# Kernel optimization log

Measured on AMD Instinct MI355X. Metric: run time of the kernel, lower is better.

Reference implementation:

```python
import jax, jax.numpy as jnp
import numpy as np

K = 3          # hypergraph neighbors (hardcoded self.kn = 3)
H = 3          # attention heads (hardcoded num_heads=3)
QKD = 32       # qkv_dim
BN_EPS = 1e-5


def _pe(channels, num_frames):
    # Ter_Embed: sinusoidal over frame index, constant across joints -> (1,C,T,1)
    pos = jnp.arange(num_frames, dtype=jnp.float32)
    div = jnp.exp(jnp.arange(0, channels, 2, dtype=jnp.float32) * (-np.log(10000.0) / channels))
    ang = pos[:, None] * div[None, :]                      # (T, C/2)
    pe = jnp.zeros((num_frames, channels), jnp.float32)
    pe = pe.at[:, 0::2].set(jnp.sin(ang)).at[:, 1::2].set(jnp.cos(ang))
    return pe.T[None, :, :, None]                          # (1,C,T,1)


def _bn(x, g, b):
    # training-mode BatchNorm2d over (N,T,V) per channel
    mu = x.mean(axis=(0, 2, 3), keepdims=True)
    var = x.var(axis=(0, 2, 3), keepdims=True)
    return (x - mu) * jax.lax.rsqrt(var + BN_EPS) * g[None, :, None, None] + b[None, :, None, None]


def setup_inputs() -> dict:
    key = jax.random.key(0)
    ks = jax.random.split(key, 16)
    N, C, T, V = 8, 128, 64, 204
    s = 0.05
    inp = {
        'x': jax.random.normal(ks[0], (N, C, T, V), jnp.float32),
        # Transform.conv1: Conv1d(k, k*k, C, groups=k) -> weight (k*k, 1, C)
        'trans_w': jax.random.normal(ks[1], (K * K, C), jnp.float32) * s,
        'trans_b': jax.random.normal(ks[2], (K * K,), jnp.float32) * s,
        # VertexConv.convK1: Conv1d(k, 1, 1)
        'convk_w': jax.random.normal(ks[3], (K,), jnp.float32) * s,
        'convk_b': jax.random.normal(ks[4], (1,), jnp.float32) * s,
        # to_qkvs: Conv2d(C, 2*H*QKD, 1)
        'qkv_w': jax.random.normal(ks[5], (2 * H * QKD, C), jnp.float32) * s,
        'qkv_b': jax.random.normal(ks[6], (2 * H * QKD,), jnp.float32) * s,
        'alphas': jnp.ones((1, H, 1, 1), jnp.float32),
        'att1s': jnp.broadcast_to(jnp.eye(T, dtype=jnp.float32), (1, H, T, T)) + 0.0,
        # out_nets: Conv2d(H*C, C, (1,1)) + BN
        'out_w': jax.random.normal(ks[7], (C, H * C), jnp.float32) * s,
        'out_b': jax.random.normal(ks[8], (C,), jnp.float32) * s,
        'out_g': jnp.ones((C,), jnp.float32) + jax.random.normal(ks[9], (C,), jnp.float32) * 0.01,
        'out_beta': jax.random.normal(ks[10], (C,), jnp.float32) * 0.01,
        # ff_net: Conv2d(C, C, 1) + BN
        'ff_w': jax.random.normal(ks[11], (C, C), jnp.float32) * s,
        'ff_b': jax.random.normal(ks[12], (C,), jnp.float32) * s,
        'ff_g': jnp.ones((C,), jnp.float32) + jax.random.normal(ks[13], (C,), jnp.float32) * 0.01,
        'ff_beta': jax.random.normal(ks[14], (C,), jnp.float32) * 0.01,
    }
    return inp


def reference(x, trans_w, trans_b, convk_w, convk_b, qkv_w, qkv_b, alphas, att1s,
              out_w, out_b, out_g, out_beta, ff_w, ff_b, ff_g, ff_beta):
    N, C, T, V = x.shape
    orign = x
    # ---------- hypergraph_knn (ssa) ----------
    # cos_dis: F.normalize over last dim (V) then contract c,t -> (N,V,V)
    nrm = jnp.linalg.norm(x, axis=-1, keepdims=True)
    xn = x / jnp.maximum(nrm, 1e-12)
    dis = jnp.einsum('nctu,nctv->nuv', xn, xn)
    _, idx = jax.lax.top_k(dis, K)                                   # (N,V,K)
    # gather neighbor feats: feats[n,c,t,v,k] = x[n,c,t,idx[n,v,k]]
    feats = jnp.take_along_axis(x[:, :, :, None, :], idx[:, None, None, :, :], axis=4)  # (N,C,T,V,K)
    # Transform: grouped Conv1d over C, group g -> K outputs
    m = feats.mean(axis=2).transpose(0, 2, 3, 1)                     # (N,V,K,C)
    mult = jnp.einsum('nvgc,gpc->nvgp', m, trans_w.reshape(K, K, C)) + trans_b.reshape(K, K)
    mult = jax.nn.softmax(mult, axis=-1)                             # (N,V,K,K)
    transformed = jnp.einsum('nctvk,nvkp->nctvp', feats, mult)
    # convK1 pools K -> 1
    pooled = jnp.einsum('nctvk,k->nctv', transformed, convk_w) + convk_b[0]
    x = jax.nn.relu(pooled + orign)
    # ---------- TTA_Block_att ----------
    xs = x + _pe(C, T)
    qkv = jnp.einsum('oc,nctv->notv', qkv_w, xs) + qkv_b[None, :, None, None]
    qkv = qkv.reshape(N, 2 * H, QKD, T, V)
    q, k = qkv[:, :H], qkv[:, H:]
    att = jnp.tanh(jnp.einsum('nhctv,nhcqv->nhtq', q, k) / (QKD * V)) * alphas + att1s  # (N,H,T,T)
    xs2 = jnp.einsum('nctv,nstq->nscqv', x, att).reshape(N, H * C, T, V)
    out = jnp.einsum('os,nstv->notv', out_w, xs2) + out_b[None, :, None, None]
    out = _bn(out, out_g, out_beta)
    xs3 = jax.nn.leaky_relu(out + x, 0.1)                            # ress is identity (in==out)
    ff = jnp.einsum('oc,nctv->notv', ff_w, xs3) + ff_b[None, :, None, None]
    ff = _bn(ff, ff_g, ff_beta)
    return jax.nn.leaky_relu(ff + x, 0.1)
```

## Files before the change

### kernel.cpp

```cpp
#include <hip/hip_runtime.h>
#include <math.h>

#define N_ 8
#define C_ 128
#define T_ 64
#define V_ 204
#define H_ 3
#define QKD_ 32
#define O2_ 192
#define TV_ 13056
#define CT_ 8192
#define TT_ 4096
#define VV_ 41616
#define NCTV_ 13369344ull
#define DSPLIT_ 32
#define ZR_ 208
#define NBLK_ 1632

typedef __attribute__((ext_vector_type(8))) short short8v;
typedef __attribute__((ext_vector_type(4))) float f32x4;

__device__ inline unsigned short bf16rnd(float f) {
  union { float f; unsigned u; } x; x.f = f;
  return (unsigned short)((x.u + 0x7FFFu + ((x.u >> 16) & 1u)) >> 16);
}
__device__ inline float bf2f(unsigned short u) {
  union { unsigned u; float f; } x; x.u = ((unsigned)u) << 16;
  return x.f;
}

__global__ void k_wprep(const float* __restrict__ qw, const float* __restrict__ ow,
                        const float* __restrict__ fw, unsigned short* __restrict__ wb) {
  int g = blockIdx.x * 256 + threadIdx.x;
  if (g >= 704 * 16) return;
  int row = g >> 4, ch = g & 15;
  const float* src;
  if (row < 192) src = qw + row * 128;
  else if (row < 576) { int r = row - 192; src = ow + (r & 127) * 384 + (r >> 7) * 128; }
  else src = fw + (row - 576) * 128;
  f32x4 a = *(const f32x4*)(src + ch * 8);
  f32x4 b = *(const f32x4*)(src + ch * 8 + 4);
  unsigned short buf[8];
  buf[0] = bf16rnd(a.x); buf[1] = bf16rnd(a.y); buf[2] = bf16rnd(a.z); buf[3] = bf16rnd(a.w);
  buf[4] = bf16rnd(b.x); buf[5] = bf16rnd(b.y); buf[6] = bf16rnd(b.z); buf[7] = bf16rnd(b.w);
  *(uint4*)(wb + (size_t)row * 128 + ch * 8) = *(const uint4*)buf;
}

__global__ void k_qkvpe(const float* __restrict__ qw, const float* __restrict__ qb,
                        float* __restrict__ qpe) {
  __shared__ float pes[C_ * T_];
  int tid = threadIdx.x;
  for (int i = tid; i < C_ * T_; i += 256) {
    int t = i & 63, c = i >> 6;
    int j = c >> 1;
    float dv = expf((2.0f * j) * (-logf(10000.0f) / (float)C_));
    float ang = (float)t * dv;
    pes[i] = (c & 1) ? cosf(ang) : sinf(ang);
  }
  __syncthreads();
  int g = blockIdx.x * 256 + tid;
  int t = g & 63, m = g >> 6;
  float a = 0.f;
  for (int c = 0; c < C_; ++c) a += qw[m * C_ + c] * pes[c * T_ + t];
  qpe[g] = a + qb[m];
}

__global__ void k_scale(const float* __restrict__ x, float* __restrict__ s) {
  int gid = blockIdx.x * blockDim.x + threadIdx.x;
  int w = gid >> 6, lane = gid & 63;
  if (w >= N_ * CT_) return;
  const f32x4* row = (const f32x4*)(x + (size_t)w * V_);
  float a = 0.f;
  for (int v4 = lane; v4 < 51; v4 += 64) {
    f32x4 t = row[v4];
    a += t.x * t.x + t.y * t.y + t.z * t.z + t.w * t.w;
  }
#pragma unroll
  for (int off = 32; off >= 1; off >>= 1) a += __shfl_down(a, off, 64);
  if (lane == 0) {
    float d = fmaxf(sqrtf(a), 1e-12f);
    s[w] = 1.0f / (d * d);
  }
}

__global__ __launch_bounds__(256) void k_zprep(const float* __restrict__ x,
                                               const float* __restrict__ s,
                                               unsigned short* __restrict__ zhi,
                                               unsigned short* __restrict__ zlo,
                                               float* __restrict__ cm) {
  int kt = blockIdx.x, ut = blockIdx.y, n = blockIdx.z;
  int k0 = kt * 64, u0 = ut * 64;
  __shared__ float Ts[64][65];
  __shared__ float sq[64];
  int tid = threadIdx.x;
  int uu = tid & 63, kk = tid >> 6;
  int u = u0 + uu;
  bool uok = u < V_;
  const float* xb = x + (size_t)n * CT_ * V_;
#pragma unroll
  for (int it = 0; it < 16; ++it) {
    int kr = kk + it * 4;
    Ts[kr][uu] = uok ? xb[(size_t)(k0 + kr) * V_ + u] : 0.f;
  }
  if (tid < 64) sq[tid] = sqrtf(s[(size_t)n * CT_ + k0 + tid]);
  __syncthreads();
  if (tid < 64 && uok) {
    float a = 0.f;
    for (int t = 0; t < 64; ++t) a += Ts[t][tid];
    cm[((size_t)n * C_ + kt) * V_ + u] = a * (1.0f / 64.0f);
  }
#pragma unroll
  for (int it = 0; it < 4; ++it) {
    int sl = tid + it * 256;
    int u_l = sl & 63, oct = (sl >> 6) & 7, half = sl >> 9;
    int ug = u0 + u_l;
    if (ug >= ZR_) continue;
    unsigned short buf[8];
    if (ug < V_) {
#pragma unroll
      for (int j = 0; j < 8; ++j) {
        float z = Ts[oct * 8 + j][u_l] * sq[oct * 8 + j];
        unsigned short h = bf16rnd(z);
        buf[j] = half ? bf16rnd(z - bf2f(h)) : h;
      }
    } else {
#pragma unroll
      for (int j = 0; j < 8; ++j) buf[j] = 0;
    }
    unsigned short* dst = (half ? zlo : zhi) +
                          (((size_t)n * 1024 + kt * 8 + oct) * ZR_ + ug) * 8;
    *(uint4*)dst = *(const uint4*)buf;
  }
}

__global__ __launch_bounds__(256) void k_dism(const unsigned short* __restrict__ zhi,
                                              const unsigned short* __restrict__ zlo,
                                              float* __restrict__ pdis) {
  int q = blockIdx.x, sp = blockIdx.y, n = blockIdx.z;
  int bu = (q == 2) ? 1 : 0, bv = (q == 0) ? 0 : 1;
  int u0 = bu * 128, v0 = bv * 128;
  bool dg = (bu == bv);
  __shared__ unsigned short As[8 * 128 * 8];
  __shared__ unsigned short Bs[8 * 128 * 8];
  int tid = threadIdx.x, lane = tid & 63, wid = tid >> 6;
  int lr = lane & 15, lg = lane >> 4;
  f32x4 acc[2][8];
#pragma unroll
  for (int mi = 0; mi < 2; ++mi)
#pragma unroll
    for (int li = 0; li < 8; ++li) acc[mi][li] = (f32x4){0.f, 0.f, 0.f, 0.f};
  const int KCH = CT_ / DSPLIT_;
  int kbase = sp * KCH, kend = kbase + KCH;
  for (int kk = kbase; kk < kend; kk += 32) {
    int koct = kk >> 3;
    __syncthreads();
#pragma unroll
    for (int it = 0; it < 4; ++it) {
      int sl = tid + it * 256;
      int row = sl & 127, hs = sl >> 7;
      int slot = hs & 3, half = hs >> 2;
      const unsigned short* src = half ? zlo : zhi;
      size_t ob = ((size_t)n * 1024 + koct + slot) * ZR_;
      int ra = u0 + row; ra = ra > 207 ? 207 : ra;
      *(uint4*)&As[(hs * 128 + row) * 8] = *(const uint4*)(src + (ob + ra) * 8);
      if (!dg) {
        int rb = v0 + row; rb = rb > 207 ? 207 : rb;
        *(uint4*)&Bs[(hs * 128 + row) * 8] = *(const uint4*)(src + (ob + rb) * 8);
      }
    }
    __syncthreads();
    const unsigned short* Bp = dg ? As : Bs;
    short8v ah[2], al[2];
#pragma unroll
    for (int mi = 0; mi < 2; ++mi) {
      int r = wid * 32 + mi * 16 + lr;
      ah[mi] = *(const short8v*)&As[(lg * 128 + r) * 8];
      al[mi] = *(const short8v*)&As[((4 + lg) * 128 + r) * 8];
    }
#pragma unroll
    for (int li = 0; li < 8; ++li) {
      int rv = li * 16 + lr;
      short8v bh = *(const short8v*)&Bp[(lg * 128 + rv) * 8];
      short8v bl = *(const short8v*)&Bp[((4 + lg) * 128 + rv) * 8];
#pragma unroll
      for (int mi = 0; mi < 2; ++mi) {
        acc[mi][li] = __builtin_amdgcn_mfma_f32_16x16x32_bf16(ah[mi], bh, acc[mi][li], 0, 0, 0);
        acc[mi][li] = __builtin_amdgcn_mfma_f32_16x16x32_bf16(ah[mi], bl, acc[mi][li], 0, 0, 0);
        acc[mi][li] = __builtin_amdgcn_mfma_f32_16x16x32_bf16(al[mi], bh, acc[mi][li], 0, 0, 0);
      }
    }
  }
  float* pb = pdis + ((size_t)sp * N_ + n) * VV_;
#pragma unroll
  for (int mi = 0; mi < 2; ++mi) {
#pragma unroll
    for (int li = 0; li < 8; ++li) {
      int v = v0 + li * 16 + lr;
      if (v >= V_) continue;
#pragma unroll
      for (int rr = 0; rr < 4; ++rr) {
        int u = u0 + wid * 32 + mi * 16 + lg * 4 + rr;
        if (u >= V_) continue;
        float val = acc[mi][li][rr];
        pb[(size_t)u * V_ + v] = val;
        if (!dg) pb[(size_t)v * V_ + u] = val;
      }
    }
  }
}

__global__ void k_topk2(const float* __restrict__ pdis, int* __restrict__ idx) {
  int r = blockIdx.x;
  int n = r / V_, u = r - n * V_;
  int lane = threadIdx.x;
  float m0 = -INFINITY, m1 = -INFINITY, m2 = -INFINITY;
  int i0 = 0x7fffffff, i1 = 0x7fffffff, i2 = 0x7fffffff;
#pragma unroll
  for (int g = 0; g < 4; ++g) {
    int v = g * 64 + lane;
    if (v >= V_) break;
    float a = 0.f;
#pragma unroll
    for (int sp = 0; sp < DSPLIT_; ++sp)
      a += pdis[((size_t)sp * N_ + n) * VV_ + (size_t)u * V_ + v];
    if (a > m0 || (a == m0 && v < i0)) {
      m2 = m1; i2 = i1; m1 = m0; i1 = i0; m0 = a; i0 = v;
    } else if (a > m1 || (a == m1 && v < i1)) {
      m2 = m1; i2 = i1; m1 = a; i1 = v;
    } else if (a > m2 || (a == m2 && v < i2)) {
      m2 = a; i2 = v;
    }
  }
#pragma unroll
  for (int msk = 1; msk < 64; msk <<= 1) {
    float o0 = __shfl_xor(m0, msk, 64), o1 = __shfl_xor(m1, msk, 64),
          o2 = __shfl_xor(m2, msk, 64);
    int p0 = __shfl_xor(i0, msk, 64), p1 = __shfl_xor(i1, msk, 64),
        p2 = __shfl_xor(i2, msk, 64);
    float ov[3] = {o0, o1, o2};
    int op[3] = {p0, p1, p2};
#pragma unroll
    for (int e = 0; e < 3; ++e) {
      float a = ov[e]; int v = op[e];
      if (a > m0 || (a == m0 && v < i0)) {
        m2 = m1; i2 = i1; m1 = m0; i1 = i0; m0 = a; i0 = v;
      } else if (a > m1 || (a == m1 && v < i1)) {
        m2 = m1; i2 = i1; m1 = a; i1 = v;
      } else if (a > m2 || (a == m2 && v < i2)) {
        m2 = a; i2 = v;
      }
    }
  }
  if (lane == 0) {
    idx[r * 3 + 0] = i0; idx[r * 3 + 1] = i1; idx[r * 3 + 2] = i2;
  }
}

__global__ void k_w2(const float* __restrict__ cm, const int* __restrict__ idx,
                     const float* __restrict__ tw, const float* __restrict__ tb,
                     const float* __restrict__ ckw, float* __restrict__ w2) {
  int r = blockIdx.x;
  int n = r / V_;
  int lane = threadIdx.x;
  __shared__ float mv[3][C_];
  const int* ib = idx + r * 3;
  int j0 = ib[0], j1 = ib[1], j2 = ib[2];
  const float* cmn = cm + (size_t)n * C_ * V_;
  for (int c = lane; c < C_; c += 64) {
    mv[0][c] = cmn[c * V_ + j0];
    mv[1][c] = cmn[c * V_ + j1];
    mv[2][c] = cmn[c * V_ + j2];
  }
  __syncthreads();
  float p[9];
#pragma unroll
  for (int gp = 0; gp < 9; ++gp) p[gp] = 0.f;
  for (int c = lane; c < C_; c += 64) {
#pragma unroll
    for (int g = 0; g < 3; ++g) {
      float m = mv[g][c];
#pragma unroll
      for (int pp = 0; pp < 3; ++pp) p[g * 3 + pp] += m * tw[(g * 3 + pp) * C_ + c];
    }
  }
#pragma unroll
  for (int off = 32; off >= 1; off >>= 1) {
#pragma unroll
    for (int gp = 0; gp < 9; ++gp) p[gp] += __shfl_down(p[gp], off, 64);
  }
  if (lane == 0) {
    float c0 = ckw[0], c1 = ckw[1], c2 = ckw[2];
#pragma unroll
    for (int g = 0; g < 3; ++g) {
      float m0 = p[g * 3 + 0] + tb[g * 3 + 0];
      float m1 = p[g * 3 + 1] + tb[g * 3 + 1];
      float m2 = p[g * 3 + 2] + tb[g * 3 + 2];
      float mx = fmaxf(m0, fmaxf(m1, m2));
      float e0 = expf(m0 - mx), e1 = expf(m1 - mx), e2 = expf(m2 - mx);
      float inv = 1.0f / (e0 + e1 + e2);
      w2[r * 3 + g] = (e0 * c0 + e1 * c1 + e2 * c2) * inv;
    }
  }
}

__global__ __launch_bounds__(256) void k_x1p(const float* __restrict__ x,
                                             const int* __restrict__ idx,
                                             const float* __restrict__ w2,
                                             const float* __restrict__ ckb,
                                             float* __restrict__ x1p,
                                             unsigned short* __restrict__ x1pb) {
  int t = blockIdx.x, ct = blockIdx.y, n = blockIdx.z;
  int c0 = ct * 32;
  __shared__ float Ts[32][209];
  __shared__ int iw[V_ * 3];
  __shared__ float ww[V_ * 3];
  int tid = threadIdx.x;
  const float* xb = x + ((size_t)n * C_ + c0) * TV_ + t * V_;
  for (int i = tid; i < 32 * V_; i += 256) {
    int c = i / V_, v = i - c * V_;
    Ts[c][v] = xb[(size_t)c * TV_ + v];
  }
  for (int i = tid; i < V_ * 3; i += 256) {
    iw[i] = idx[(size_t)n * V_ * 3 + i];
    ww[i] = w2[(size_t)n * V_ * 3 + i];
  }
  __syncthreads();
  float cb = ckb[0];
  for (int i = tid; i < 32 * V_; i += 256) {
    int v = i >> 5, cl = i & 31;
    int b = v * 3;
    float pooled = Ts[cl][iw[b]] * ww[b] + Ts[cl][iw[b + 1]] * ww[b + 1] +
                   Ts[cl][iw[b + 2]] * ww[b + 2] + cb;
    float val = fmaxf(pooled + Ts[cl][v], 0.f);
    size_t o = ((size_t)(n * V_ + v) * T_ + t) * C_ + c0 + cl;
    x1p[o] = val;
    x1pb[o] = bf16rnd(val);
  }
}

template <int MCH, int OBF, int STATS>
__global__ __launch_bounds__(256) void k_gmm2(const unsigned short* __restrict__ Wb,
                                              const unsigned short* __restrict__ Xp,
                                              const float* __restrict__ addv,
                                              void* __restrict__ Yv,
                                              float* __restrict__ part) {
  int l0 = blockIdx.x * 128, n = blockIdx.z;
  __shared__ unsigned short Xs[128 * 136];
  __shared__ unsigned short Ys[64 * 128];
  int tid = threadIdx.x, lane = tid & 63, wid = tid >> 6;
  int wm = wid >> 1, wl = wid & 1;
  int lr = lane & 15, lg = lane >> 4;
  const unsigned short* xb = Xp + ((size_t)n * TV_ + l0) * 128;
#pragma unroll
  for (int it = 0; it < 8; ++it) {
    int g = tid + it * 256;
    int row = g >> 4, ch = g & 15;
    *(uint4*)&Xs[row * 136 + ch * 8] = *(const uint4*)(xb + (size_t)row * 128 + ch * 8);
  }
  __syncthreads();
  for (int mc = 0; mc < MCH; ++mc) {
    short8v a[2][4];
#pragma unroll
    for (int mi = 0; mi < 2; ++mi) {
      int m = mc * 64 + wm * 32 + mi * 16 + lr;
#pragma unroll
      for (int ks = 0; ks < 4; ++ks)
        a[mi][ks] = *(const short8v*)(Wb + (size_t)m * 128 + ks * 32 + lg * 8);
    }
    f32x4 acc[2][4];
#pragma unroll
    for (int mi = 0; mi < 2; ++mi)
#pragma unroll
      for (int li = 0; li < 4; ++li) acc[mi][li] = (f32x4){0.f, 0.f, 0.f, 0.f};
#pragma unroll
    for (int ks = 0; ks < 4; ++ks) {
#pragma unroll
      for (int li = 0; li < 4; ++li) {
        short8v b = *(const short8v*)&Xs[(wl * 64 + li * 16 + lr) * 136 + ks * 32 + lg * 8];
#pragma unroll
        for (int mi = 0; mi < 2; ++mi)
          acc[mi][li] = __builtin_amdgcn_mfma_f32_16x16x32_bf16(a[mi][ks], b, acc[mi][li], 0, 0, 0);
      }
    }
    if (OBF) {
      __syncthreads();
#pragma unroll
      for (int mi = 0; mi < 2; ++mi)
#pragma unroll
        for (int li = 0; li < 4; ++li) {
          int lloc = wl * 64 + li * 16 + lr;
          int tt = (l0 + lloc) & 63;
#pragma unroll
          for (int r = 0; r < 4; ++r) {
            int mloc = wm * 32 + mi * 16 + lg * 4 + r;
            float val = acc[mi][li][r] + addv[(mc * 64 + mloc) * 64 + tt];
            Ys[mloc * 128 + lloc] = bf16rnd(val);
          }
        }
      __syncthreads();
      unsigned short* Yh = (unsigned short*)Yv;
#pragma unroll
      for (int it = 0; it < 4; ++it) {
        int g = tid + it * 256;
        int row = g >> 4, ch = g & 15;
        *(uint4*)(Yh + ((size_t)n * O2_ + mc * 64 + row) * TV_ + l0 + ch * 8) =
            *(const uint4*)&Ys[row * 128 + ch * 8];
      }
    } else {
      float* Yf = (float*)Yv;
      float st1[2][4] = {}, st2[2][4] = {};
#pragma unroll
      for (int mi = 0; mi < 2; ++mi)
#pragma unroll
        for (int li = 0; li < 4; ++li) {
          int lp = l0 + wl * 64 + li * 16 + lr;
          int m = mc * 64 + wm * 32 + mi * 16 + lg * 4;
          f32x4 o;
#pragma unroll
          for (int r = 0; r < 4; ++r) {
            o[r] = acc[mi][li][r] + addv[m + r];
            if (STATS) { st1[mi][r] += o[r]; st2[mi][r] += o[r] * o[r]; }
          }
          *(f32x4*)(Yf + ((size_t)n * TV_ + lp) * 128 + m) = o;
        }
      if (STATS) {
        int blk2 = ((n * gridDim.x + blockIdx.x) * 2 + wl) * 256;
#pragma unroll
        for (int mi = 0; mi < 2; ++mi)
#pragma unroll
          for (int r = 0; r < 4; ++r) {
            float a1 = st1[mi][r], a2 = st2[mi][r];
            a1 += __shfl_xor(a1, 1, 64); a2 += __shfl_xor(a2, 1, 64);
            a1 += __shfl_xor(a1, 2, 64); a2 += __shfl_xor(a2, 2, 64);
            a1 += __shfl_xor(a1, 4, 64); a2 += __shfl_xor(a2, 4, 64);
            a1 += __shfl_xor(a1, 8, 64); a2 += __shfl_xor(a2, 8, 64);
            if (lr == 0) {
              int m = mc * 64 + wm * 32 + mi * 16 + lg * 4 + r;
              part[blk2 + m] = a1;
              part[blk2 + 128 + m] = a2;
            }
          }
      }
    }
  }
}

__global__ __launch_bounds__(256) void k_att(const unsigned short* __restrict__ qkv,
                                             float* __restrict__ attp) {
  int cp = blockIdx.x, h = blockIdx.y, n = blockIdx.z;
  __shared__ float Qs[102][68], Ks[102][68];
  int tid = threadIdx.x;
  int ty = tid >> 4, tx = tid & 15;
  float acc[4][4] = {};
  for (int cc = 0; cc < 2; ++cc) {
    int c = cp * 2 + cc;
    const unsigned short* qb = qkv + ((size_t)n * O2_ + h * QKD_ + c) * TV_;
    const unsigned short* kb = qkv + ((size_t)n * O2_ + H_ * QKD_ + h * QKD_ + c) * TV_;
    for (int vh = 0; vh < 2; ++vh) {
      for (int g = tid; g < 816; g += 256) {
        int v = g >> 3, t0 = (g & 7) * 8;
        uint4 qv = *(const uint4*)(qb + vh * 6528 + g * 8);
        uint4 kv = *(const uint4*)(kb + vh * 6528 + g * 8);
        const unsigned short* qs = (const unsigned short*)&qv;
        const unsigned short* ks2 = (const unsigned short*)&kv;
#pragma unroll
        for (int j = 0; j < 8; ++j) {
          Qs[v][t0 + j] = bf2f(qs[j]);
          Ks[v][t0 + j] = bf2f(ks2[j]);
        }
      }
      __syncthreads();
      for (int vv = 0; vv < 102; ++vv) {
        f32x4 qa = *(const f32x4*)&Qs[vv][ty * 4];
        f32x4 ka = *(const f32x4*)&Ks[vv][tx * 4];
#pragma unroll
        for (int i = 0; i < 4; ++i)
#pragma unroll
          for (int j = 0; j < 4; ++j) acc[i][j] += qa[i] * ka[j];
      }
      __syncthreads();
    }
  }
  float* ar = attp + (((size_t)cp * N_ + n) * H_ + h) * TT_;
#pragma unroll
  for (int i = 0; i < 4; ++i)
#pragma unroll
    for (int j = 0; j < 4; ++j)
      ar[(ty * 4 + i) * T_ + tx * 4 + j] = acc[i][j];
}

__global__ void k_attfin(const float* __restrict__ attp, const float* __restrict__ alphas,
                         const float* __restrict__ att1s, unsigned short* __restrict__ attT) {
  int i = blockIdx.x * blockDim.x + threadIdx.x;
  if (i >= N_ * H_ * TT_) return;
  int tt = i % TT_;
  int h = (i / TT_) % H_;
  int n = i / (H_ * TT_);
  float raw = 0.f;
#pragma unroll
  for (int cp = 0; cp < 16; ++cp)
    raw += attp[(((size_t)cp * N_ + n) * H_ + h) * TT_ + tt];
  int t = tt >> 6, q = tt & 63;
  float v = tanhf(raw * (1.0f / 6528.0f)) * alphas[h] + att1s[h * TT_ + tt];
  attT[(size_t)(n * 64 + q) * 192 + h * 64 + t] = bf16rnd(v);
}

__global__ __launch_bounds__(256) void k_fcomb(const unsigned short* __restrict__ x1pb,
                                               const unsigned short* __restrict__ w3b,
                                               const unsigned short* __restrict__ attT,
                                               const float* __restrict__ outb,
                                               float* __restrict__ op,
                                               float* __restrict__ part) {
  int v = blockIdx.x, n = blockIdx.z;
  __shared__ unsigned short Yv[128 * 72];
  int tid = threadIdx.x, lane = tid & 63, wid = tid >> 6;
  int lr = lane & 15, lg = lane >> 4;
  const unsigned short* xb = x1pb + ((size_t)(n * V_ + v) * T_) * 128;
  f32x4 acc2[4][2];
#pragma unroll
  for (int mq = 0; mq < 4; ++mq)
#pragma unroll
    for (int oi = 0; oi < 2; ++oi) acc2[mq][oi] = (f32x4){0.f, 0.f, 0.f, 0.f};
  const unsigned short* ab = attT + (size_t)n * 64 * 192;
  for (int h = 0; h < H_; ++h) {
    short8v a1[2][4];
#pragma unroll
    for (int mi = 0; mi < 2; ++mi) {
      int m = wid * 32 + mi * 16 + lr;
#pragma unroll
      for (int ks = 0; ks < 4; ++ks)
        a1[mi][ks] = *(const short8v*)(w3b + ((size_t)(h * 128 + m)) * 128 + ks * 32 + lg * 8);
    }
    f32x4 acc1[2][4];
#pragma unroll
    for (int mi = 0; mi < 2; ++mi)
#pragma unroll
      for (int li = 0; li < 4; ++li) acc1[mi][li] = (f32x4){0.f, 0.f, 0.f, 0.f};
#pragma unroll
    for (int ks = 0; ks < 4; ++ks) {
#pragma unroll
      for (int li = 0; li < 4; ++li) {
        short8v b = *(const short8v*)(xb + (size_t)(li * 16 + lr) * 128 + ks * 32 + lg * 8);
#pragma unroll
        for (int mi = 0; mi < 2; ++mi)
          acc1[mi][li] = __builtin_amdgcn_mfma_f32_16x16x32_bf16(a1[mi][ks], b, acc1[mi][li], 0, 0, 0);
      }
    }
    __syncthreads();
#pragma unroll
    for (int mi = 0; mi < 2; ++mi)
#pragma unroll
      for (int li = 0; li < 4; ++li) {
        int t = li * 16 + lr;
#pragma unroll
        for (int r = 0; r < 4; ++r) {
          int o = wid * 32 + mi * 16 + lg * 4 + r;
          Yv[o * 72 + t] = bf16rnd(acc1[mi][li][r]);
        }
      }
    __syncthreads();
#pragma unroll
    for (int ks2 = 0; ks2 < 2; ++ks2) {
      short8v bY[2];
#pragma unroll
      for (int oi = 0; oi < 2; ++oi)
        bY[oi] = *(const short8v*)&Yv[(wid * 32 + oi * 16 + lr) * 72 + ks2 * 32 + lg * 8];
#pragma unroll
      for (int mq = 0; mq < 4; ++mq) {
        short8v a2 = *(const short8v*)(ab + (size_t)(mq * 16 + lr) * 192 + h * 64 + ks2 * 32 + lg * 8);
#pragma unroll
        for (int oi = 0; oi < 2; ++oi)
          acc2[mq][oi] = __builtin_amdgcn_mfma_f32_16x16x32_bf16(a2, bY[oi], acc2[mq][oi], 0, 0, 0);
      }
    }
  }
  float s1[2] = {0.f, 0.f}, s2[2] = {0.f, 0.f};
#pragma unroll
  for (int mq = 0; mq < 4; ++mq)
#pragma unroll
    for (int oi = 0; oi < 2; ++oi) {
      int o = wid * 32 + oi * 16 + lr;
      float bo = outb[o];
#pragma unroll
      for (int r = 0; r < 4; ++r) {
        int q = mq * 16 + lg * 4 + r;
        float val = acc2[mq][oi][r] + bo;
        op[((size_t)(n * V_ + v) * T_ + q) * 128 + o] = val;
        s1[oi] += val; s2[oi] += val * val;
      }
    }
  int blk = (n * V_ + v) * 256;
#pragma unroll
  for (int oi = 0; oi < 2; ++oi) {
    float a1 = s1[oi], a2 = s2[oi];
    a1 += __shfl_xor(a1, 16, 64); a2 += __shfl_xor(a2, 16, 64);
    a1 += __shfl_xor(a1, 32, 64); a2 += __shfl_xor(a2, 32, 64);
    if ((lane & 48) == 0) {
      int o = wid * 32 + oi * 16 + lr;
      part[blk + o] = a1;
      part[blk + 128 + o] = a2;
    }
  }
}

__global__ void k_bnab(const float* __restrict__ part, const float* __restrict__ g,
                       const float* __restrict__ beta, float* __restrict__ ab) {
  int c = blockIdx.x;
  int tid = threadIdx.x;
  float s1 = 0.f, s2 = 0.f;
  for (int b = tid; b < NBLK_; b += 256) {
    s1 += part[b * 256 + c];
    s2 += part[b * 256 + 128 + c];
  }
  __shared__ float r1[256], r2[256];
  r1[tid] = s1; r2[tid] = s2;
  __syncthreads();
  for (int off = 128; off >= 1; off >>= 1) {
    if (tid < off) { r1[tid] += r1[tid + off]; r2[tid] += r2[tid + off]; }
    __syncthreads();
  }
  if (tid == 0) {
    const float cnt = (float)(N_ * TV_);
    float mu = r1[0] / cnt;
    float rstd = rsqrtf(r2[0] / cnt - mu * mu + 1e-5f);
    float a = rstd * g[c];
    ab[c] = a;
    ab[128 + c] = beta[c] - mu * a;
  }
}

__global__ void k_bnxt(const float* __restrict__ op, const float* __restrict__ x1p,
                       const float* __restrict__ ab, unsigned short* __restrict__ xt) {
  __shared__ float sa[128], sb[128];
  int tid = threadIdx.x;
  if (tid < 128) { sa[tid] = ab[tid]; sb[tid] = ab[128 + tid]; }
  __syncthreads();
  const unsigned NU = (unsigned)(NCTV_ / 8);
  const f32x4* o4 = (const f32x4*)op;
  const f32x4* r4 = (const f32x4*)x1p;
  for (unsigned u = blockIdx.x * 256u + tid; u < NU; u += gridDim.x * 256u) {
    unsigned row = u >> 4, ch = u & 15;
    unsigned bi = row * 32 + ch * 2;
    f32x4 v0 = o4[bi], v1 = o4[bi + 1];
    f32x4 q0 = r4[bi], q1 = r4[bi + 1];
    int c8 = ch * 8;
    unsigned short buf[8];
#pragma unroll
    for (int j = 0; j < 4; ++j) {
      float t0 = v0[j] * sa[c8 + j] + sb[c8 + j] + q0[j];
      float t1 = v1[j] * sa[c8 + 4 + j] + sb[c8 + 4 + j] + q1[j];
      buf[j] = bf16rnd(t0 > 0.f ? t0 : 0.1f * t0);
      buf[4 + j] = bf16rnd(t1 > 0.f ? t1 : 0.1f * t1);
    }
    *(uint4*)(xt + (size_t)u * 8) = *(const uint4*)buf;
  }
}

__global__ __launch_bounds__(256) void k_bnfinal(const float* __restrict__ ff,
                                                 const float* __restrict__ x1p,
                                                 const float* __restrict__ ab,
                                                 float* __restrict__ dout) {
  int ct = blockIdx.x, t = blockIdx.y, n = blockIdx.z;
  int c0 = ct * 32;
  __shared__ float Tf[V_][33];
  __shared__ float sa[32], sb[32];
  int tid = threadIdx.x;
  if (tid < 32) { sa[tid] = ab[c0 + tid]; sb[tid] = ab[128 + c0 + tid]; }
  __syncthreads();
  for (int i = tid; i < V_ * 32; i += 256) {
    int v = i >> 5, cl = i & 31;
    size_t a = ((size_t)(n * V_ + v) * T_ + t) * 128 + c0 + cl;
    float val = ff[a] * sa[cl] + sb[cl] + x1p[a];
    Tf[v][cl] = val > 0.f ? val : 0.1f * val;
  }
  __syncthreads();
  for (int i = tid; i < 32 * V_; i += 256) {
    int cl = i / V_, v = i - cl * V_;
    dout[((size_t)(n * C_ + c0 + cl) * T_ + t) * V_ + v] = Tf[v][cl];
  }
}

extern "C" void kernel_launch(void* const* d_in, const int* in_sizes, int n_in,
                              void* d_out, int out_size, void* d_ws, size_t ws_size,
                              hipStream_t stream) {
  (void)in_sizes; (void)n_in; (void)out_size; (void)ws_size;
  const float* x        = (const float*)d_in[0];
  const float* trans_w  = (const float*)d_in[1];
  const float* trans_b  = (const float*)d_in[2];
  const float* convk_w  = (const float*)d_in[3];
  const float* convk_b  = (const float*)d_in[4];
  const float* qkv_w    = (const float*)d_in[5];
  const float* qkv_b    = (const float*)d_in[6];
  const float* alphas   = (const float*)d_in[7];
  const float* att1s    = (const float*)d_in[8];
  const float* out_w    = (const float*)d_in[9];
  const float* out_b    = (const float*)d_in[10];
  const float* out_g    = (const float*)d_in[11];
  const float* out_beta = (const float*)d_in[12];
  const float* ff_w     = (const float*)d_in[13];
  const float* ff_b     = (const float*)d_in[14];
  const float* ff_g     = (const float*)d_in[15];
  const float* ff_beta  = (const float*)d_in[16];

  float* ws = (float*)d_ws;
  size_t off = 0;
  float* x1p  = ws + off; off += NCTV_;
  float* big  = ws + off; off += (size_t)N_ * O2_ * TV_ / 2;
  float* pre  = ws + off; off += NCTV_;
  float* sbuf = ws + off; off += (size_t)N_ * CT_;
  int*   idx  = (int*)(ws + off); off += (size_t)N_ * V_ * 3 + 4;
  float* cm   = ws + off; off += (size_t)N_ * C_ * V_;
  float* w2   = ws + off; off += (size_t)N_ * V_ * 3 + 4;
  float* attp = ws + off; off += (size_t)16 * N_ * H_ * TT_;
  unsigned short* attT = (unsigned short*)(ws + off); off += (size_t)N_ * 64 * 192 / 2;
  float* part = ws + off; off += (size_t)NBLK_ * 256;
  float* ab   = ws + off; off += 512;
  float* qpe  = ws + off; off += (size_t)O2_ * T_;
  unsigned short* wb = (unsigned short*)(ws + off); off += 704 * 128 / 2;
  const size_t ZEL = (size_t)N_ * 1024 * ZR_ * 8;
  unsigned short* zhi = (unsigned short*)(ws + off);
  unsigned short* zlo = zhi + ZEL;
  off += ZEL;
  unsigned short* x1pb  = zhi;
  unsigned short* xs3pb = zlo;
  unsigned short* qkvb  = (unsigned short*)big;
  float* dout = (float*)d_out;

  k_wprep<<<44, 256, 0, stream>>>(qkv_w, out_w, ff_w, wb);
  k_qkvpe<<<48, 256, 0, stream>>>(qkv_w, qkv_b, qpe);
  k_scale<<<(N_ * CT_ * 64) / 256, 256, 0, stream>>>(x, sbuf);
  k_zprep<<<dim3(128, 4, N_), 256, 0, stream>>>(x, sbuf, zhi, zlo, cm);
  k_dism<<<dim3(3, DSPLIT_, N_), 256, 0, stream>>>(zhi, zlo, pre);
  k_topk2<<<N_ * V_, 64, 0, stream>>>(pre, idx);
  k_w2<<<N_ * V_, 64, 0, stream>>>(cm, idx, trans_w, trans_b, convk_w, w2);
  k_x1p<<<dim3(64, 4, N_), 256, 0, stream>>>(x, idx, w2, convk_b, x1p, x1pb);

  k_gmm2<3, 1, 0><<<dim3(102, 1, N_), 256, 0, stream>>>(wb, x1pb, qpe, qkvb, nullptr);
  k_att<<<dim3(16, H_, N_), 256, 0, stream>>>(qkvb, attp);
  k_attfin<<<384, 256, 0, stream>>>(attp, alphas, att1s, attT);

  k_fcomb<<<dim3(204, 1, N_), 256, 0, stream>>>(x1pb, wb + 192 * 128, attT, out_b, pre, part);

  k_bnab<<<128, 256, 0, stream>>>(part, out_g, out_beta, ab);
  k_bnxt<<<2048, 256, 0, stream>>>(pre, x1p, ab, xs3pb);

  k_gmm2<2, 0, 1><<<dim3(102, 1, N_), 256, 0, stream>>>(wb + 576 * 128, xs3pb, ff_b, pre, part);
  k_bnab<<<128, 256, 0, stream>>>(part, ff_g, ff_beta, ab + 256);
  k_bnfinal<<<dim3(4, 64, N_), 256, 0, stream>>>(pre, x1p, ab + 256, dout);
}
```

Before: 364.1 us.

## Store intermediate activations in bf16 and hoist fcomb B-fragments into registers

Drops the fp32 copies of x1p and the pre-BN output buffers and keeps only bf16 versions. Downstream elementwise BN kernels now read bf16, which cuts global memory traffic roughly in half. k_fcomb keeps the x1p B fragments in registers across heads and double-buffers its shared tile to remove one barrier per head. It also stages its output through LDS for coalesced bf16 stores. The trade-off is lower precision on the residual and BN inputs, plus higher register pressure in k_fcomb.

```diff
diff --git a/kernel.cpp b/kernel.cpp
--- a/kernel.cpp
+++ b/kernel.cpp
@@ -307,7 +307,6 @@
                                              const int* __restrict__ idx,
                                              const float* __restrict__ w2,
                                              const float* __restrict__ ckb,
-                                             float* __restrict__ x1p,
                                              unsigned short* __restrict__ x1pb) {
   int t = blockIdx.x, ct = blockIdx.y, n = blockIdx.z;
   int c0 = ct * 32;
@@ -332,9 +331,7 @@
     float pooled = Ts[cl][iw[b]] * ww[b] + Ts[cl][iw[b + 1]] * ww[b + 1] +
                    Ts[cl][iw[b + 2]] * ww[b + 2] + cb;
     float val = fmaxf(pooled + Ts[cl][v], 0.f);
-    size_t o = ((size_t)(n * V_ + v) * T_ + t) * C_ + c0 + cl;
-    x1p[o] = val;
-    x1pb[o] = bf16rnd(val);
+    x1pb[((size_t)(n * V_ + v) * T_ + t) * C_ + c0 + cl] = bf16rnd(val);
   }
 }
 
@@ -407,7 +404,7 @@
             *(const uint4*)&Ys[row * 128 + ch * 8];
       }
     } else {
-      float* Yf = (float*)Yv;
+      unsigned short* Yh = (unsigned short*)Yv;
       float st1[2][4] = {}, st2[2][4] = {};
 #pragma unroll
       for (int mi = 0; mi < 2; ++mi)
@@ -415,13 +412,14 @@
         for (int li = 0; li < 4; ++li) {
           int lp = l0 + wl * 64 + li * 16 + lr;
           int m = mc * 64 + wm * 32 + mi * 16 + lg * 4;
-          f32x4 o;
+          unsigned short b4[4];
 #pragma unroll
           for (int r = 0; r < 4; ++r) {
-            o[r] = acc[mi][li][r] + addv[m + r];
-            if (STATS) { st1[mi][r] += o[r]; st2[mi][r] += o[r] * o[r]; }
+            float val = acc[mi][li][r] + addv[m + r];
+            if (STATS) { st1[mi][r] += val; st2[mi][r] += val * val; }
+            b4[r] = bf16rnd(val);
           }
-          *(f32x4*)(Yf + ((size_t)n * TV_ + lp) * 128 + m) = o;
+          *(uint2*)(Yh + ((size_t)n * TV_ + lp) * 128 + m) = *(const uint2*)b4;
         }
       if (STATS) {
         int blk2 = ((n * gridDim.x + blockIdx.x) * 2 + wl) * 256;
@@ -509,13 +507,19 @@
                                                const unsigned short* __restrict__ w3b,
                                                const unsigned short* __restrict__ attT,
                                                const float* __restrict__ outb,
-                                               float* __restrict__ op,
+                                               unsigned short* __restrict__ preb,
                                                float* __restrict__ part) {
   int v = blockIdx.x, n = blockIdx.z;
-  __shared__ unsigned short Yv[128 * 72];
+  __shared__ unsigned short Yv[2][128 * 68];
   int tid = threadIdx.x, lane = tid & 63, wid = tid >> 6;
   int lr = lane & 15, lg = lane >> 4;
   const unsigned short* xb = x1pb + ((size_t)(n * V_ + v) * T_) * 128;
+  short8v bx[4][4];
+#pragma unroll
+  for (int ks = 0; ks < 4; ++ks)
+#pragma unroll
+    for (int li = 0; li < 4; ++li)
+      bx[ks][li] = *(const short8v*)(xb + (size_t)(li * 16 + lr) * 128 + ks * 32 + lg * 8);
   f32x4 acc2[4][2];
 #pragma unroll
   for (int mq = 0; mq < 4; ++mq)
@@ -523,6 +527,7 @@
     for (int oi = 0; oi < 2; ++oi) acc2[mq][oi] = (f32x4){0.f, 0.f, 0.f, 0.f};
   const unsigned short* ab = attT + (size_t)n * 64 * 192;
   for (int h = 0; h < H_; ++h) {
+    unsigned short* Yc = Yv[h & 1];
     short8v a1[2][4];
 #pragma unroll
     for (int mi = 0; mi < 2; ++mi) {
@@ -537,16 +542,13 @@
 #pragma unroll
       for (int li = 0; li < 4; ++li) acc1[mi][li] = (f32x4){0.f, 0.f, 0.f, 0.f};
 #pragma unroll
-    for (int ks = 0; ks < 4; ++ks) {
-#pragma unroll
-      for (int li = 0; li < 4; ++li) {
-        short8v b = *(const short8v*)(xb + (size_t)(li * 16 + lr) * 128 + ks * 32 + lg * 8);
+    for (int ks = 0; ks < 4; ++ks)
+#pragma unroll
+      for (int li = 0; li < 4; ++li)
 #pragma unroll
         for (int mi = 0; mi < 2; ++mi)
-          acc1[mi][li] = __builtin_amdgcn_mfma_f32_16x16x32_bf16(a1[mi][ks], b, acc1[mi][li], 0, 0, 0);
-      }
-    }
-    __syncthreads();
+          acc1[mi][li] = __builtin_amdgcn_mfma_f32_16x16x32_bf16(a1[mi][ks], bx[ks][li],
+                                                                 acc1[mi][li], 0, 0, 0);
 #pragma unroll
     for (int mi = 0; mi < 2; ++mi)
 #pragma unroll
@@ -555,7 +557,7 @@
 #pragma unroll
         for (int r = 0; r < 4; ++r) {
           int o = wid * 32 + mi * 16 + lg * 4 + r;
-          Yv[o * 72 + t] = bf16rnd(acc1[mi][li][r]);
+          Yc[o * 68 + t] = bf16rnd(acc1[mi][li][r]);
         }
       }
     __syncthreads();
@@ -564,7 +566,7 @@
       short8v bY[2];
 #pragma unroll
       for (int oi = 0; oi < 2; ++oi)
-        bY[oi] = *(const short8v*)&Yv[(wid * 32 + oi * 16 + lr) * 72 + ks2 * 32 + lg * 8];
+        bY[oi] = *(const short8v*)&Yc[(wid * 32 + oi * 16 + lr) * 68 + ks2 * 32 + lg * 8];
 #pragma unroll
       for (int mq = 0; mq < 4; ++mq) {
         short8v a2 = *(const short8v*)(ab + (size_t)(mq * 16 + lr) * 192 + h * 64 + ks2 * 32 + lg * 8);
@@ -574,6 +576,7 @@
       }
     }
   }
+  unsigned short* Ys2 = Yv[1];
   float s1[2] = {0.f, 0.f}, s2[2] = {0.f, 0.f};
 #pragma unroll
   for (int mq = 0; mq < 4; ++mq)
@@ -585,8 +588,8 @@
       for (int r = 0; r < 4; ++r) {
         int q = mq * 16 + lg * 4 + r;
         float val = acc2[mq][oi][r] + bo;
-        op[((size_t)(n * V_ + v) * T_ + q) * 128 + o] = val;
         s1[oi] += val; s2[oi] += val * val;
+        Ys2[q * 136 + o] = bf16rnd(val);
       }
     }
   int blk = (n * V_ + v) * 256;
@@ -601,6 +604,14 @@
       part[blk + 128 + o] = a2;
     }
   }
+  __syncthreads();
+  unsigned short* ob2 = preb + ((size_t)(n * V_ + v) * T_) * 128;
+#pragma unroll
+  for (int it = 0; it < 4; ++it) {
+    int g = tid + it * 256;
+    int row = g >> 4, ch = g & 15;
+    *(uint4*)(ob2 + (size_t)row * 128 + ch * 8) = *(const uint4*)&Ys2[row * 136 + ch * 8];
+  }
 }
 
 __global__ void k_bnab(const float* __restrict__ part, const float* __restrict__ g,
@@ -629,35 +640,33 @@
   }
 }
 
-__global__ void k_bnxt(const float* __restrict__ op, const float* __restrict__ x1p,
+__global__ void k_bnxt(const unsigned short* __restrict__ preb,
+                       const unsigned short* __restrict__ x1pb,
                        const float* __restrict__ ab, unsigned short* __restrict__ xt) {
   __shared__ float sa[128], sb[128];
   int tid = threadIdx.x;
   if (tid < 128) { sa[tid] = ab[tid]; sb[tid] = ab[128 + tid]; }
   __syncthreads();
   const unsigned NU = (unsigned)(NCTV_ / 8);
-  const f32x4* o4 = (const f32x4*)op;
-  const f32x4* r4 = (const f32x4*)x1p;
+  const uint4* p4 = (const uint4*)preb;
+  const uint4* r4 = (const uint4*)x1pb;
   for (unsigned u = blockIdx.x * 256u + tid; u < NU; u += gridDim.x * 256u) {
-    unsigned row = u >> 4, ch = u & 15;
-    unsigned bi = row * 32 + ch * 2;
-    f32x4 v0 = o4[bi], v1 = o4[bi + 1];
-    f32x4 q0 = r4[bi], q1 = r4[bi + 1];
-    int c8 = ch * 8;
+    int c8 = (u & 15) * 8;
+    uint4 pv = p4[u], rv = r4[u];
+    const unsigned short* ps = (const unsigned short*)&pv;
+    const unsigned short* rs = (const unsigned short*)&rv;
     unsigned short buf[8];
 #pragma unroll
-    for (int j = 0; j < 4; ++j) {
-      float t0 = v0[j] * sa[c8 + j] + sb[c8 + j] + q0[j];
-      float t1 = v1[j] * sa[c8 + 4 + j] + sb[c8 + 4 + j] + q1[j];
-      buf[j] = bf16rnd(t0 > 0.f ? t0 : 0.1f * t0);
-      buf[4 + j] = bf16rnd(t1 > 0.f ? t1 : 0.1f * t1);
+    for (int j = 0; j < 8; ++j) {
+      float t = bf2f(ps[j]) * sa[c8 + j] + sb[c8 + j] + bf2f(rs[j]);
+      buf[j] = bf16rnd(t > 0.f ? t : 0.1f * t);
     }
     *(uint4*)(xt + (size_t)u * 8) = *(const uint4*)buf;
   }
 }
 
-__global__ __launch_bounds__(256) void k_bnfinal(const float* __restrict__ ff,
-                                                 const float* __restrict__ x1p,
+__global__ __launch_bounds__(256) void k_bnfinal(const unsigned short* __restrict__ preb,
+                                                 const unsigned short* __restrict__ x1pb,
                                                  const float* __restrict__ ab,
                                                  float* __restrict__ dout) {
   int ct = blockIdx.x, t = blockIdx.y, n = blockIdx.z;
@@ -667,11 +676,19 @@
   int tid = threadIdx.x;
   if (tid < 32) { sa[tid] = ab[c0 + tid]; sb[tid] = ab[128 + c0 + tid]; }
   __syncthreads();
-  for (int i = tid; i < V_ * 32; i += 256) {
-    int v = i >> 5, cl = i & 31;
-    size_t a = ((size_t)(n * V_ + v) * T_ + t) * 128 + c0 + cl;
-    float val = ff[a] * sa[cl] + sb[cl] + x1p[a];
-    Tf[v][cl] = val > 0.f ? val : 0.1f * val;
+  for (int i = tid; i < V_ * 4; i += 256) {
+    int v = i >> 2, ch = i & 3;
+    size_t a = ((size_t)(n * V_ + v) * T_ + t) * 128 + c0 + ch * 8;
+    uint4 pv = *(const uint4*)(preb + a);
+    uint4 rv = *(const uint4*)(x1pb + a);
+    const unsigned short* ps = (const unsigned short*)&pv;
+    const unsigned short* rs = (const unsigned short*)&rv;
+#pragma unroll
+    for (int j = 0; j < 8; ++j) {
+      int cl = ch * 8 + j;
+      float val = bf2f(ps[j]) * sa[cl] + sb[cl] + bf2f(rs[j]);
+      Tf[v][cl] = val > 0.f ? val : 0.1f * val;
+    }
   }
   __syncthreads();
   for (int i = tid; i < 32 * V_; i += 256) {
@@ -704,9 +721,10 @@
 
   float* ws = (float*)d_ws;
   size_t off = 0;
-  float* x1p  = ws + off; off += NCTV_;
-  float* big  = ws + off; off += (size_t)N_ * O2_ * TV_ / 2;
-  float* pre  = ws + off; off += NCTV_;
+  float* gq = ws + off; off += (size_t)N_ * O2_ * TV_ / 2 + NCTV_ / 2;
+  float* pdis = gq;
+  unsigned short* qkvb = (unsigned short*)gq;
+  unsigned short* preb = (unsigned short*)(gq + (size_t)N_ * O2_ * TV_ / 2);
   float* sbuf = ws + off; off += (size_t)N_ * CT_;
   int*   idx  = (int*)(ws + off); off += (size_t)N_ * V_ * 3 + 4;
   float* cm   = ws + off; off += (size_t)N_ * C_ * V_;
@@ -723,28 +741,27 @@
   off += ZEL;
   unsigned short* x1pb  = zhi;
   unsigned short* xs3pb = zlo;
-  unsigned short* qkvb  = (unsigned short*)big;
   float* dout = (float*)d_out;
 
   k_wprep<<<44, 256, 0, stream>>>(qkv_w, out_w, ff_w, wb);
   k_qkvpe<<<48, 256, 0, stream>>>(qkv_w, qkv_b, qpe);
   k_scale<<<(N_ * CT_ * 64) / 256, 256, 0, stream>>>(x, sbuf);
   k_zprep<<<dim3(128, 4, N_), 256, 0, stream>>>(x, sbuf, zhi, zlo, cm);
-  k_dism<<<dim3(3, DSPLIT_, N_), 256, 0, stream>>>(zhi, zlo, pre);
-  k_topk2<<<N_ * V_, 64, 0, stream>>>(pre, idx);
+  k_dism<<<dim3(3, DSPLIT_, N_), 256, 0, stream>>>(zhi, zlo, pdis);
+  k_topk2<<<N_ * V_, 64, 0, stream>>>(pdis, idx);
   k_w2<<<N_ * V_, 64, 0, stream>>>(cm, idx, trans_w, trans_b, convk_w, w2);
-  k_x1p<<<dim3(64, 4, N_), 256, 0, stream>>>(x, idx, w2, convk_b, x1p, x1pb);
+  k_x1p<<<dim3(64, 4, N_), 256, 0, stream>>>(x, idx, w2, convk_b, x1pb);
 
   k_gmm2<3, 1, 0><<<dim3(102, 1, N_), 256, 0, stream>>>(wb, x1pb, qpe, qkvb, nullptr);
   k_att<<<dim3(16, H_, N_), 256, 0, stream>>>(qkvb, attp);
   k_attfin<<<384, 256, 0, stream>>>(attp, alphas, att1s, attT);
 
-  k_fcomb<<<dim3(204, 1, N_), 256, 0, stream>>>(x1pb, wb + 192 * 128, attT, out_b, pre, part);
+  k_fcomb<<<dim3(204, 1, N_), 256, 0, stream>>>(x1pb, wb + 192 * 128, attT, out_b, preb, part);
 
   k_bnab<<<128, 256, 0, stream>>>(part, out_g, out_beta, ab);
-  k_bnxt<<<2048, 256, 0, stream>>>(pre, x1p, ab, xs3pb);
-
-  k_gmm2<2, 0, 1><<<dim3(102, 1, N_), 256, 0, stream>>>(wb + 576 * 128, xs3pb, ff_b, pre, part);
+  k_bnxt<<<2048, 256, 0, stream>>>(preb, x1pb, ab, xs3pb);
+
+  k_gmm2<2, 0, 1><<<dim3(102, 1, N_), 256, 0, stream>>>(wb + 576 * 128, xs3pb, ff_b, preb, part);
   k_bnab<<<128, 256, 0, stream>>>(part, ff_g, ff_beta, ab + 256);
-  k_bnfinal<<<dim3(4, 64, N_), 256, 0, stream>>>(pre, x1p, ab + 256, dout);
-}
+  k_bnfinal<<<dim3(4, 64, N_), 256, 0, stream>>>(preb, x1pb, ab + 256, dout);
+}
```

After: 323.6 us. 11.1% less time.
